# Kernel tuning notes

Measured on AMD Instinct MI355X. Metric: run time of the kernel, lower is better.

## Reference

```python
import jax, jax.numpy as jnp
import numpy as np
import math

B, C, H, W = 512, 64, 8, 8
E, NH, MEM = 64, 8, 8          # embed_dim, num_heads, mem_n
HD = E // NH                   # head_dim
THD = H * W * HD               # tot_head_dim = 512
AMB = 5.0                      # attn_mask_b
LN_EPS = 1e-5


def conv2d(x, w, b):
    y = jax.lax.conv_general_dilated(x, w, (1, 1), 'SAME',
                                     dimension_numbers=('NCHW', 'OIHW', 'NCHW'))
    return y + b[None, :, None, None]


def setup_inputs() -> dict:
    key = jax.random.key(0)
    ks = jax.random.split(key, 14)
    r = lambda k, s, sc=1.0: jax.random.normal(k, s, dtype=jnp.float32) * sc
    return {
        'input': r(ks[0], (B, C, H, W)),
        'h_cur': r(ks[1], (B, E, H, W)),
        'c_cur': r(ks[2], (B, E, H, W)),
        'concat_k': r(ks[3], (B, MEM, NH, THD)),
        'concat_v': r(ks[4], (B, MEM, NH, THD)),
        'attn_mask': jax.random.randint(ks[5], (B * NH, 1, MEM), 0, 2).astype(bool),
        'conv_w': r(ks[6], (5 * E, C + E, 3, 3), 0.05),
        'conv_b': jnp.zeros((5 * E,), jnp.float32),
        'proj_w': r(ks[7], (3 * E, C, 3, 3), 0.05),
        'proj_b': jnp.zeros((3 * E,), jnp.float32),
        'out_w': r(ks[8], (E, E, 3, 3), 0.05),
        'out_b': jnp.zeros((E,), jnp.float32),
        'ln_w': jnp.ones((E, H, W), jnp.float32),
        'ln_b': jnp.zeros((E, H, W), jnp.float32),
        'pos_w': r(ks[9], (MEM, H * W * E), 0.02),
        'pos_b': jax.random.uniform(ks[10], (MEM, NH), jnp.float32, -0.1, 0.1),
    }


def _cell(input, h_cur, c_cur, concat_k, concat_v, attn_mask,
          conv_w, conv_b, proj_w, proj_b, out_w, out_b, ln_w, ln_b, pos_w, pos_b):
    # ConvLSTM gates
    combined = jnp.concatenate([input, h_cur], axis=1)          # [B, C+E, H, W]
    cc = conv2d(combined, conv_w, conv_b)                       # [B, 5E, H, W]
    cc_i, cc_f, cc_o, cc_g, cc_a = jnp.split(cc, 5, axis=1)
    i = jax.nn.sigmoid(cc_i)
    f = jax.nn.sigmoid(cc_f)
    o = jax.nn.sigmoid(cc_o)
    g = jnp.tanh(cc_g)
    a = jax.nn.sigmoid(cc_a)
    c_next = f * c_cur + i * g

    # attention over growing memory
    kqv = conv2d(input, proj_w, proj_b)                         # [B, 3E, H, W]
    k, q, v = jnp.split(kqv, 3, axis=1)
    # [B, E, H, W] -> [B*NH, 1, THD] (contiguous split of E into NH heads)
    resh = lambda x: x.reshape(B * NH, 1, THD)
    k, q, v = resh(k), resh(q), resh(v)
    q_scaled = q / math.sqrt(THD)

    # prior memory: [B, MEM, NH, THD] -> [B*NH, MEM-1, THD]
    def mem_resh(m):
        return jnp.transpose(m[:, 1:], (1, 0, 2, 3)).reshape(MEM - 1, B * NH, THD).transpose(1, 0, 2)
    k_full = jnp.concatenate([mem_resh(concat_k), k], axis=1)   # [B*NH, MEM, THD]
    v_full = jnp.concatenate([mem_resh(concat_v), v], axis=1)

    # learned positional key offsets / score biases
    pos_w_e = jnp.broadcast_to(pos_w[:, None, :], (MEM, B, H * W * E)) \
                 .reshape(MEM, B * NH, THD).transpose(1, 0, 2)  # [B*NH, MEM, THD]
    pos_b_e = jnp.broadcast_to(pos_b[:, None, :], (MEM, B, NH)) \
                 .reshape(MEM, B * NH).T                        # [B*NH, MEM]
    k_full = k_full + pos_w_e

    # additive mask: -inf where masked, last slot forced to +attn_mask_b
    mask = jnp.where(attn_mask, -jnp.inf, 0.0).astype(q.dtype)  # [B*NH, 1, MEM]
    mask = mask.at[:, :, -1].set(AMB)

    scores = mask + jnp.einsum('bqd,bkd->bqk', q_scaled, k_full) + pos_b_e[:, None, :]
    w = jax.nn.softmax(scores, axis=-1)                         # [B*NH, 1, MEM]
    attn = jnp.einsum('bqk,bkd->bqd', w, v_full)                # [B*NH, 1, THD]
    attn = attn.reshape(B, E, H, W)

    out = conv2d(attn, out_w, out_b) + input[:, :E]
    # LayerNorm over (E, H, W)
    mu = jnp.mean(out, axis=(1, 2, 3), keepdims=True)
    var = jnp.mean((out - mu) ** 2, axis=(1, 2, 3), keepdims=True)
    out = (out - mu) / jnp.sqrt(var + LN_EPS) * ln_w[None] + ln_b[None]

    c_next = c_next + a * jnp.tanh(out)
    h_next = o * jnp.tanh(c_next)

    ret = lambda m: m.transpose(1, 0, 2).reshape(MEM, B, NH, THD).transpose(1, 0, 2, 3)
    return h_next, c_next, ret(k_full), ret(v_full)


def reference(input, h_cur, c_cur, concat_k, concat_v, attn_mask,
              conv_w, conv_b, proj_w, proj_b, out_w, out_b, ln_w, ln_b, pos_w, pos_b):
    return _cell(input, h_cur, c_cur, concat_k, concat_v, attn_mask,
                 conv_w, conv_b, proj_w, proj_b, out_w, out_b, ln_w, ln_b, pos_w, pos_b)
```

## Files before the change

kernel.cpp:

```cpp
#include <hip/hip_runtime.h>

typedef short short8 __attribute__((ext_vector_type(8)));
typedef __bf16 bf16x8 __attribute__((ext_vector_type(8)));
typedef float f32x4 __attribute__((ext_vector_type(4)));
typedef short s16x4 __attribute__((ext_vector_type(4)));
typedef unsigned u32x4 __attribute__((ext_vector_type(4)));

__device__ __forceinline__ short f2bf(float f) {
  unsigned u = __builtin_bit_cast(unsigned, f);
  u = (u + 0x7FFFu + ((u >> 16) & 1u)) >> 16;
  return (short)u;
}
__device__ __forceinline__ f32x4 mfma16(short8 a, short8 b, f32x4 c) {
  return __builtin_amdgcn_mfma_f32_16x16x32_bf16(
      __builtin_bit_cast(bf16x8, a), __builtin_bit_cast(bf16x8, b), c, 0, 0, 0);
}
__device__ __forceinline__ float sigm(float x) { return 1.0f / (1.0f + __expf(-x)); }
__device__ __forceinline__ float ftanh(float x) {
  return 1.0f - 2.0f / (1.0f + __expf(2.0f * x));
}
__device__ __forceinline__ f32x4 ld4(const float* p) { return *(const f32x4*)p; }
__device__ __forceinline__ void ntst4(float* p, f32x4 v) {
  __builtin_nontemporal_store(v, (f32x4*)p);
}

__global__ void pack_w(const float* __restrict__ w1, const float* __restrict__ w2,
                       const float* __restrict__ w3, short* __restrict__ out) {
  int e = blockIdx.x * 256 + threadIdx.x;
  if (e < 46080) {
    int kb8 = e / 320, n = e % 320;
    short8 v;
#pragma unroll
    for (int j = 0; j < 8; ++j) {
      int k = kb8 * 8 + j;
      int tap = k >> 7, ci = k & 127;
      v[j] = f2bf(w1[(n * 128 + ci) * 9 + tap]);
    }
    *(short8*)&out[e * 8] = v;
    return;
  }
  e -= 46080;
  if (e < 13824) {
    int kb8 = e / 192, n = e % 192;
    short8 v;
#pragma unroll
    for (int j = 0; j < 8; ++j) {
      int k = kb8 * 8 + j;
      int tap = k >> 6, ci = k & 63;
      v[j] = f2bf(w2[(n * 64 + ci) * 9 + tap]);
    }
    *(short8*)&out[(46080 + e) * 8] = v;
    return;
  }
  e -= 13824;
  {
    int kb8 = e / 64, n = e % 64;
    short8 v;
#pragma unroll
    for (int j = 0; j < 8; ++j) {
      int k = kb8 * 8 + j;
      int tap = k >> 6, ci = k & 63;
      v[j] = f2bf(w3[(n * 64 + ci) * 9 + tap]);
    }
    *(short8*)&out[(46080 + 13824 + e) * 8] = v;
  }
}

__launch_bounds__(512, 4)
__global__ void mid2_k(const float* __restrict__ input, const float* __restrict__ h_cur,
                       const float* __restrict__ c_cur, const float* __restrict__ ck,
                       const int* __restrict__ amask,
                       const float* __restrict__ conv_b, const float* __restrict__ proj_b,
                       const float* __restrict__ pos_w, const float* __restrict__ pos_b,
                       const short* __restrict__ pk1, const short* __restrict__ pk2,
                       float* __restrict__ o_k, float* __restrict__ o_v,
                       float* __restrict__ ws_wt, float* __restrict__ ws_ct,
                       unsigned* __restrict__ ws_oa) {
  __shared__ short comb[12800];
  __shared__ float Xb[4160];
  __shared__ float Vx[4160];
  __shared__ float sc_lds[8];
  float* combf = (float*)comb;
  unsigned* Xbu = (unsigned*)Xb;

  const int tid = threadIdx.x;
  const int wave = tid >> 6, lane = tid & 63;
  const int col = lane & 15, g4 = lane >> 4;
  const int wc = wave >> 1, wm = wave & 1;
  const int ch = wc * 16 + col;

  if (blockIdx.x < 512) {
    const int b = blockIdx.x;
    const int hd = wave;
    const int d0 = lane * 4, d1 = (lane + 64) * 4;
    if (tid < 8) sc_lds[tid] = 0.f;

#pragma unroll
    for (int i = 0; i < 2; ++i) {
      int idx = (tid + 512 * i) * 4;
      int c = idx >> 6, p0 = idx & 63;
      f32x4 vi = ld4(&input[b * 4096 + idx]);
#pragma unroll
      for (int j = 0; j < 4; ++j) {
        int p = p0 + j;
        int pp = ((p >> 3) + 1) * 10 + (p & 7) + 1;
        comb[pp * 64 + ((c + pp * 8) & 63)] = f2bf(vi[j]);
      }
    }
    for (int i = tid; i < 2304; i += 512) {
      int pr = i >> 6, c = i & 63;
      int pp = (pr < 10) ? pr
               : (pr < 20) ? (80 + pr)
               : (pr < 28) ? ((pr - 19) * 10)
                           : ((pr - 27) * 10 + 9);
      comb[pp * 64 + c] = 0;
    }
    __syncthreads();

    f32x4 acc2[2][3];
#pragma unroll
    for (int m = 0; m < 2; ++m)
#pragma unroll
      for (int g = 0; g < 3; ++g) acc2[m][g] = (f32x4){0.f, 0.f, 0.f, 0.f};
    short8 bb2[3];
#pragma unroll
    for (int g = 0; g < 3; ++g)
      bb2[g] = *(const short8*)&pk2[((g4)*192 + g * 64 + ch) * 8];
    for (int s = 0; s < 18; ++s) {
      short8 bbn[3];
      if (s < 17) {
        int kb8 = (s + 1) * 4 + g4;
#pragma unroll
        for (int g = 0; g < 3; ++g)
          bbn[g] = *(const short8*)&pk2[(kb8 * 192 + g * 64 + ch) * 8];
      }
      int tap = s >> 1, cib = s & 1;
      int kh = tap / 3, kw = tap % 3;
      short8 a[2];
#pragma unroll
      for (int m = 0; m < 2; ++m) {
        int p = (wm * 2 + m) * 16 + col;
        int pp = ((p >> 3) + kh) * 10 + (p & 7) + kw;
        int slot = (cib * 32 + g4 * 8 + pp * 8) & 63;
        a[m] = *(const short8*)&comb[pp * 64 + slot];
      }
#pragma unroll
      for (int m = 0; m < 2; ++m)
#pragma unroll
        for (int g = 0; g < 3; ++g) acc2[m][g] = mfma16(a[m], bb2[g], acc2[m][g]);
      if (s < 17) {
#pragma unroll
        for (int g = 0; g < 3; ++g) bb2[g] = bbn[g];
      }
    }

    float kreg[8], qreg[8], vreg[8], part7 = 0.f;
    {
      float pb0 = proj_b[ch], pb1 = proj_b[64 + ch], pb2 = proj_b[128 + ch];
      const float rsq = 0.044194173824159216f;
#pragma unroll
      for (int m = 0; m < 2; ++m)
#pragma unroll
        for (int r = 0; r < 4; ++r) {
          int p = (wm * 2 + m) * 16 + g4 * 4 + r;
          float kf = acc2[m][0][r] + pb0 + pos_w[7 * 4096 + ch * 64 + p];
          float qf = (acc2[m][1][r] + pb1) * rsq;
          float vf = acc2[m][2][r] + pb2;
          kreg[m * 4 + r] = kf;
          qreg[m * 4 + r] = qf;
          vreg[m * 4 + r] = vf;
          part7 = fmaf(qf, kf, part7);
        }
    }
    atomicAdd(&sc_lds[ch >> 3], part7);

    int msks[7];
    float pbv[7];
#pragma unroll
    for (int m = 0; m < 7; ++m) {
      msks[m] = amask[(b * 8 + hd) * 8 + m];
      pbv[m] = pos_b[m * 8 + hd];
    }

    __syncthreads();

#pragma unroll
    for (int m = 0; m < 2; ++m)
#pragma unroll
      for (int r = 0; r < 4; ++r) {
        int p = (wm * 2 + m) * 16 + g4 * 4 + r;
        combf[ch * 65 + p] = kreg[m * 4 + r];
        Xb[ch * 65 + p] = qreg[m * 4 + r];
        Vx[ch * 65 + p] = vreg[m * 4 + r];
      }
    __syncthreads();

    const size_t base7 = (size_t)(b * 64 + 56) * 512;
#pragma unroll
    for (int i = 0; i < 2; ++i) {
      int idx = (tid + 512 * i) * 4;
      int c = idx >> 6, p0 = idx & 63;
      f32x4 kq, vq;
#pragma unroll
      for (int j = 0; j < 4; ++j) {
        kq[j] = combf[c * 65 + p0 + j];
        vq[j] = Vx[c * 65 + p0 + j];
      }
      ntst4(&o_k[base7 + idx], kq);
      *(f32x4*)&o_v[base7 + idx] = vq;
    }
    const int cs0 = d0 >> 6, po0 = d0 & 63, cs1 = d1 >> 6, po1 = d1 & 63;
    f32x4 q0, q1;
#pragma unroll
    for (int j = 0; j < 4; ++j) {
      q0[j] = Xb[(hd * 8 + cs0) * 65 + po0 + j];
      q1[j] = Xb[(hd * 8 + cs1) * 65 + po1 + j];
    }
    float sc7 = sc_lds[hd] + pos_b[7 * 8 + hd] + 5.0f;

    float scv[8];
    scv[7] = sc7;
#pragma unroll
    for (int m = 0; m < 7; ++m) {
      const float* kp = ck + ((size_t)((b * 8 + m + 1) * 8 + hd)) * 512;
      const float* pw = pos_w + m * 4096 + hd * 512;
      f32x4 k0 = ld4(kp + d0) + ld4(pw + d0);
      f32x4 k1 = ld4(kp + d1) + ld4(pw + d1);
      float* dst = o_k + ((size_t)((b * 8 + m) * 8 + hd)) * 512;
      ntst4(dst + d0, k0);
      ntst4(dst + d1, k1);
      float part = 0.f;
#pragma unroll
      for (int j = 0; j < 4; ++j) {
        part = fmaf(q0[j], k0[j], part);
        part = fmaf(q1[j], k1[j], part);
      }
#pragma unroll
      for (int off = 32; off >= 1; off >>= 1) part += __shfl_xor(part, off);
      scv[m] = part + pbv[m] + (msks[m] ? -__builtin_inff() : 0.0f);
    }

    float mx = scv[0];
#pragma unroll
    for (int m = 1; m < 8; ++m) mx = fmaxf(mx, scv[m]);
    float w[8], s = 0.f;
#pragma unroll
    for (int m = 0; m < 8; ++m) {
      w[m] = __expf(scv[m] - mx);
      s += w[m];
    }
    float inv = 1.0f / s;
    if (lane == 0) {
#pragma unroll
      for (int m = 0; m < 8; ++m)
        ws_wt[(size_t)b * 64 + hd * 8 + m] = w[m] * inv;
    }
  } else {
    const int b = blockIdx.x - 512;
#pragma unroll
    for (int i = 0; i < 2; ++i) {
      int idx = (tid + 512 * i) * 4;
      int c = idx >> 6, p0 = idx & 63;
      f32x4 vi = ld4(&input[b * 4096 + idx]);
      f32x4 vh = ld4(&h_cur[b * 4096 + idx]);
      f32x4 vc = ld4(&c_cur[b * 4096 + idx]);
#pragma unroll
      for (int j = 0; j < 4; ++j) {
        int p = p0 + j;
        int pp = ((p >> 3) + 1) * 10 + (p & 7) + 1;
        comb[pp * 128 + ((c + pp * 8) & 127)] = f2bf(vi[j]);
        comb[pp * 128 + ((c + 64 + pp * 8) & 127)] = f2bf(vh[j]);
        Xb[c * 65 + p] = vc[j];
      }
    }
    for (int i = tid; i < 4608; i += 512) {
      int pr = i >> 7, c = i & 127;
      int pp = (pr < 10) ? pr
               : (pr < 20) ? (80 + pr)
               : (pr < 28) ? ((pr - 19) * 10)
                           : ((pr - 27) * 10 + 9);
      comb[pp * 128 + c] = 0;
    }
    __syncthreads();

    f32x4 acc1[2][5];
#pragma unroll
    for (int m = 0; m < 2; ++m)
#pragma unroll
      for (int g = 0; g < 5; ++g) acc1[m][g] = (f32x4){0.f, 0.f, 0.f, 0.f};
    short8 bb1[5];
#pragma unroll
    for (int g = 0; g < 5; ++g)
      bb1[g] = *(const short8*)&pk1[((g4)*320 + g * 64 + ch) * 8];
    for (int s = 0; s < 36; ++s) {
      short8 bbn[5];
      if (s < 35) {
        int kb8 = (s + 1) * 4 + g4;
#pragma unroll
        for (int g = 0; g < 5; ++g)
          bbn[g] = *(const short8*)&pk1[(kb8 * 320 + g * 64 + ch) * 8];
      }
      int tap = s >> 2, cib = s & 3;
      int kh = tap / 3, kw = tap % 3;
      short8 a[2];
#pragma unroll
      for (int m = 0; m < 2; ++m) {
        int p = (wm * 2 + m) * 16 + col;
        int pp = ((p >> 3) + kh) * 10 + (p & 7) + kw;
        int slot = (cib * 32 + g4 * 8 + pp * 8) & 127;
        a[m] = *(const short8*)&comb[pp * 128 + slot];
      }
#pragma unroll
      for (int m = 0; m < 2; ++m)
#pragma unroll
        for (int g = 0; g < 5; ++g) acc1[m][g] = mfma16(a[m], bb1[g], acc1[m][g]);
      if (s < 35) {
#pragma unroll
        for (int g = 0; g < 5; ++g) bb1[g] = bbn[g];
      }
    }

    float ctv[8];
    unsigned oav[8];
    {
      float bi0 = conv_b[ch], bi1 = conv_b[64 + ch], bi2 = conv_b[128 + ch];
      float bi3 = conv_b[192 + ch], bi4 = conv_b[256 + ch];
#pragma unroll
      for (int m = 0; m < 2; ++m)
#pragma unroll
        for (int r = 0; r < 4; ++r) {
          int p = (wm * 2 + m) * 16 + g4 * 4 + r;
          float iv = sigm(acc1[m][0][r] + bi0);
          float fv = sigm(acc1[m][1][r] + bi1);
          float ov = sigm(acc1[m][2][r] + bi2);
          float gv = ftanh(acc1[m][3][r] + bi3);
          float av = sigm(acc1[m][4][r] + bi4);
          ctv[m * 4 + r] = fv * Xb[ch * 65 + p] + iv * gv;
          oav[m * 4 + r] = ((unsigned)(unsigned short)f2bf(av) << 16) |
                           (unsigned)(unsigned short)f2bf(ov);
        }
    }
    __syncthreads();
#pragma unroll
    for (int m = 0; m < 2; ++m)
#pragma unroll
      for (int r = 0; r < 4; ++r) {
        int p = (wm * 2 + m) * 16 + g4 * 4 + r;
        combf[ch * 65 + p] = ctv[m * 4 + r];
        Xbu[ch * 65 + p] = oav[m * 4 + r];
      }
    __syncthreads();
#pragma unroll
    for (int i = 0; i < 2; ++i) {
      int idx = (tid + 512 * i) * 4;
      int c = idx >> 6, p0 = idx & 63;
      f32x4 cq;
      u32x4 oq;
#pragma unroll
      for (int j = 0; j < 4; ++j) {
        cq[j] = combf[c * 65 + p0 + j];
        oq[j] = Xbu[c * 65 + p0 + j];
      }
      *(f32x4*)&ws_ct[(size_t)b * 4096 + idx] = cq;
      *(u32x4*)&ws_oa[(size_t)b * 4096 + idx] = oq;
    }
  }
}

__launch_bounds__(512, 4)
__global__ void tail_k(const float* __restrict__ input, const float* __restrict__ cv,
                       const float* __restrict__ ws_wt,
                       const float* __restrict__ ws_ct,
                       const unsigned* __restrict__ ws_oa,
                       const float* __restrict__ out_b,
                       const float* __restrict__ ln_w, const float* __restrict__ ln_b,
                       const short* __restrict__ pk3,
                       float* __restrict__ o_h, float* __restrict__ o_c,
                       float* __restrict__ o_v) {
  __shared__ short comb[8320];
  __shared__ float Xb[4160];
  __shared__ float wt_s[64];
  __shared__ float red[16];
  float* combf = (float*)comb;
  unsigned* Xbu = (unsigned*)Xb;

  const int b = blockIdx.x;
  const int tid = threadIdx.x;
  const int wave = tid >> 6, lane = tid & 63;
  const int col = lane & 15, g4 = lane >> 4;
  const int wc = wave >> 1, wm = wave & 1;
  const int ch = wc * 16 + col;
  const int hd = wave;
  const int d0 = lane * 4, d1 = (lane + 64) * 4;

  f32x4 ctr[2];
  u32x4 oar[2];
#pragma unroll
  for (int i = 0; i < 2; ++i) {
    int idx = (tid + 512 * i) * 4;
    ctr[i] = ld4(&ws_ct[(size_t)b * 4096 + idx]);
    oar[i] = *(const u32x4*)&ws_oa[(size_t)b * 4096 + idx];
  }
  if (tid < 64) wt_s[tid] = ws_wt[(size_t)b * 64 + tid];

#pragma unroll
  for (int i = 0; i < 2; ++i) {
    int idx = (tid + 512 * i) * 4;
    int c = idx >> 6, p0 = idx & 63;
    f32x4 vi = ld4(&input[b * 4096 + idx]);
#pragma unroll
    for (int j = 0; j < 4; ++j) Xb[c * 65 + p0 + j] = vi[j];
  }
  for (int i = tid; i < 2304; i += 512) {
    int pr = i >> 6, c = i & 63;
    int pp = (pr < 10) ? pr
             : (pr < 20) ? (80 + pr)
             : (pr < 28) ? ((pr - 19) * 10)
                         : ((pr - 27) * 10 + 9);
    comb[pp * 64 + c] = 0;
  }
  __syncthreads();

  float wv[8];
#pragma unroll
  for (int m = 0; m < 8; ++m) wv[m] = wt_s[hd * 8 + m];

  f32x4 a0 = (f32x4){0.f, 0.f, 0.f, 0.f};
  f32x4 a1 = (f32x4){0.f, 0.f, 0.f, 0.f};
#pragma unroll
  for (int m = 0; m < 7; ++m) {
    const float* vp = cv + ((size_t)((b * 8 + m + 1) * 8 + hd)) * 512;
    f32x4 v0 = ld4(vp + d0);
    f32x4 v1 = ld4(vp + d1);
    float* dst = o_v + ((size_t)((b * 8 + m) * 8 + hd)) * 512;
    ntst4(dst + d0, v0);
    ntst4(dst + d1, v1);
    a0 += v0 * wv[m];
    a1 += v1 * wv[m];
  }
  {
    const float* vp = o_v + ((size_t)((b * 8 + 7) * 8 + hd)) * 512;
    a0 += ld4(vp + d0) * wv[7];
    a1 += ld4(vp + d1) * wv[7];
  }
#pragma unroll
  for (int j = 0; j < 4; ++j) {
    int dA = d0 + j, dB = d1 + j;
    int cA = hd * 8 + (dA >> 6), pA = dA & 63;
    int cB = hd * 8 + (dB >> 6), pB = dB & 63;
    int ppA = ((pA >> 3) + 1) * 10 + (pA & 7) + 1;
    int ppB = ((pB >> 3) + 1) * 10 + (pB & 7) + 1;
    comb[ppA * 64 + ((cA + ppA * 8) & 63)] = f2bf(a0[j]);
    comb[ppB * 64 + ((cB + ppB * 8) & 63)] = f2bf(a1[j]);
  }
  __syncthreads();

  f32x4 acc3[2];
  acc3[0] = (f32x4){0.f, 0.f, 0.f, 0.f};
  acc3[1] = (f32x4){0.f, 0.f, 0.f, 0.f};
  short8 bb3 = *(const short8*)&pk3[((g4)*64 + ch) * 8];
  for (int s = 0; s < 18; ++s) {
    short8 bbn;
    if (s < 17) {
      int kb8 = (s + 1) * 4 + g4;
      bbn = *(const short8*)&pk3[(kb8 * 64 + ch) * 8];
    }
    int tap = s >> 1, cib = s & 1;
    int kh = tap / 3, kw = tap % 3;
    short8 a[2];
#pragma unroll
    for (int m = 0; m < 2; ++m) {
      int p = (wm * 2 + m) * 16 + col;
      int pp = ((p >> 3) + kh) * 10 + (p & 7) + kw;
      int slot = (cib * 32 + g4 * 8 + pp * 8) & 63;
      a[m] = *(const short8*)&comb[pp * 64 + slot];
    }
#pragma unroll
    for (int m = 0; m < 2; ++m) acc3[m] = mfma16(a[m], bb3, acc3[m]);
    if (s < 17) bb3 = bbn;
  }

  float ov_[8], s1 = 0.f, s2 = 0.f;
  {
    float ob = out_b[ch];
#pragma unroll
    for (int m = 0; m < 2; ++m)
#pragma unroll
      for (int r = 0; r < 4; ++r) {
        int p = (wm * 2 + m) * 16 + g4 * 4 + r;
        float v = acc3[m][r] + ob + Xb[ch * 65 + p];
        ov_[m * 4 + r] = v;
        s1 += v;
        s2 += v * v;
      }
  }
#pragma unroll
  for (int off = 32; off >= 1; off >>= 1) {
    s1 += __shfl_xor(s1, off);
    s2 += __shfl_xor(s2, off);
  }
  if (lane == 0) { red[wave] = s1; red[8 + wave] = s2; }
  __syncthreads();
  float ts1 = 0.f, ts2 = 0.f;
#pragma unroll
  for (int w = 0; w < 8; ++w) { ts1 += red[w]; ts2 += red[8 + w]; }
  float mu = ts1 * (1.0f / 4096.0f);
  float var = ts2 * (1.0f / 4096.0f) - mu * mu;
  float rstd = rsqrtf(var + 1e-5f);

#pragma unroll
  for (int i = 0; i < 2; ++i) {
    int idx = (tid + 512 * i) * 4;
    int c = idx >> 6, p0 = idx & 63;
#pragma unroll
    for (int j = 0; j < 4; ++j) {
      combf[c * 65 + p0 + j] = ctr[i][j];
      Xbu[c * 65 + p0 + j] = oar[i][j];
    }
  }
  __syncthreads();

#pragma unroll
  for (int m = 0; m < 2; ++m)
#pragma unroll
    for (int r = 0; r < 4; ++r) {
      int p = (wm * 2 + m) * 16 + g4 * 4 + r;
      float ct = combf[ch * 65 + p];
      unsigned u = Xbu[ch * 65 + p];
      float og = __builtin_bit_cast(float, u << 16);
      float ag = __builtin_bit_cast(float, u & 0xffff0000u);
      float oln = (ov_[m * 4 + r] - mu) * rstd * ln_w[ch * 64 + p] + ln_b[ch * 64 + p];
      float cn = ct + ag * ftanh(oln);
      float hv = og * ftanh(cn);
      combf[ch * 65 + p] = hv;
      Xb[ch * 65 + p] = cn;
    }
  __syncthreads();
#pragma unroll
  for (int i = 0; i < 2; ++i) {
    int idx = (tid + 512 * i) * 4;
    int c = idx >> 6, p0 = idx & 63;
    f32x4 hq, cq;
#pragma unroll
    for (int j = 0; j < 4; ++j) {
      hq[j] = combf[c * 65 + p0 + j];
      cq[j] = Xb[c * 65 + p0 + j];
    }
    *(f32x4*)&o_h[b * 4096 + idx] = hq;
    *(f32x4*)&o_c[b * 4096 + idx] = cq;
  }
}

__launch_bounds__(512, 4)
__global__ void kqv_k(const float* __restrict__ input,
                      const float* __restrict__ proj_b,
                      const float* __restrict__ pos_w,
                      const short* __restrict__ pk2,
                      float* __restrict__ q_out, float* __restrict__ o_k,
                      float* __restrict__ o_v) {
  __shared__ short comb[6400];
  __shared__ float Xk[4160], Xq[4160], Xv[4160];
  const int b = blockIdx.x;
  const int tid = threadIdx.x;
  const int wave = tid >> 6, lane = tid & 63;
  const int col = lane & 15, g4 = lane >> 4;
  const int wc = wave >> 1, wm = wave & 1;
  const int ch = wc * 16 + col;
#pragma unroll
  for (int i = 0; i < 2; ++i) {
    int idx = (tid + 512 * i) * 4;
    int c = idx >> 6, p0 = idx & 63;
    f32x4 vi = ld4(&input[b * 4096 + idx]);
#pragma unroll
    for (int j = 0; j < 4; ++j) {
      int p = p0 + j;
      int pp = ((p >> 3) + 1) * 10 + (p & 7) + 1;
      comb[pp * 64 + ((c + pp * 8) & 63)] = f2bf(vi[j]);
    }
  }
  for (int i = tid; i < 2304; i += 512) {
    int pr = i >> 6, c = i & 63;
    int pp = (pr < 10) ? pr
             : (pr < 20) ? (80 + pr)
             : (pr < 28) ? ((pr - 19) * 10)
                         : ((pr - 27) * 10 + 9);
    comb[pp * 64 + c] = 0;
  }
  __syncthreads();
  f32x4 acc2[2][3];
#pragma unroll
  for (int m = 0; m < 2; ++m)
#pragma unroll
    for (int g = 0; g < 3; ++g) acc2[m][g] = (f32x4){0.f, 0.f, 0.f, 0.f};
  short8 bb2[3];
#pragma unroll
  for (int g = 0; g < 3; ++g)
    bb2[g] = *(const short8*)&pk2[((g4)*192 + g * 64 + ch) * 8];
  for (int s = 0; s < 18; ++s) {
    short8 bbn[3];
    if (s < 17) {
      int kb8 = (s + 1) * 4 + g4;
#pragma unroll
      for (int g = 0; g < 3; ++g)
        bbn[g] = *(const short8*)&pk2[(kb8 * 192 + g * 64 + ch) * 8];
    }
    int tap = s >> 1, cib = s & 1;
    int kh = tap / 3, kw = tap % 3;
    short8 a[2];
#pragma unroll
    for (int m = 0; m < 2; ++m) {
      int p = (wm * 2 + m) * 16 + col;
      int pp = ((p >> 3) + kh) * 10 + (p & 7) + kw;
      int slot = (cib * 32 + g4 * 8 + pp * 8) & 63;
      a[m] = *(const short8*)&comb[pp * 64 + slot];
    }
#pragma unroll
    for (int m = 0; m < 2; ++m)
#pragma unroll
      for (int g = 0; g < 3; ++g) acc2[m][g] = mfma16(a[m], bb2[g], acc2[m][g]);
    if (s < 17) {
#pragma unroll
      for (int g = 0; g < 3; ++g) bb2[g] = bbn[g];
    }
  }
  {
    float pb0 = proj_b[ch], pb1 = proj_b[64 + ch], pb2 = proj_b[128 + ch];
    const float rsq = 0.044194173824159216f;
#pragma unroll
    for (int m = 0; m < 2; ++m)
#pragma unroll
      for (int r = 0; r < 4; ++r) {
        int p = (wm * 2 + m) * 16 + g4 * 4 + r;
        Xk[ch * 65 + p] = acc2[m][0][r] + pb0 + pos_w[7 * 4096 + ch * 64 + p];
        Xq[ch * 65 + p] = (acc2[m][1][r] + pb1) * rsq;
        Xv[ch * 65 + p] = acc2[m][2][r] + pb2;
      }
  }
  __syncthreads();
  const size_t base7 = (size_t)(b * 64 + 56) * 512;
#pragma unroll
  for (int i = 0; i < 2; ++i) {
    int idx = (tid + 512 * i) * 4;
    int c = idx >> 6, p0 = idx & 63;
    f32x4 kq, qq, vq;
#pragma unroll
    for (int j = 0; j < 4; ++j) {
      kq[j] = Xk[c * 65 + p0 + j];
      qq[j] = Xq[c * 65 + p0 + j];
      vq[j] = Xv[c * 65 + p0 + j];
    }
    *(f32x4*)&o_k[base7 + idx] = kq;
    *(f32x4*)&q_out[(size_t)b * 4096 + idx] = qq;
    *(f32x4*)&o_v[base7 + idx] = vq;
  }
}

__launch_bounds__(64, 4)
__global__ void attn_k(const float* __restrict__ ck, const float* __restrict__ cv,
                       const int* __restrict__ amask,
                       const float* __restrict__ pos_w,
                       const float* __restrict__ pos_b,
                       const float* __restrict__ q_in,
                       float* __restrict__ o_k, float* __restrict__ o_v,
                       float* __restrict__ attn_out) {
  const int b = blockIdx.x >> 3;
  const int hd = blockIdx.x & 7;
  const int lane = threadIdx.x;
  const int d0 = lane * 4, d1 = (lane + 64) * 4;
  const float* qp = q_in + (size_t)b * 4096 + hd * 512;
  f32x4 q0 = ld4(qp + d0);
  f32x4 q1 = ld4(qp + d1);
  float sc[8];
#pragma unroll
  for (int m = 0; m < 7; ++m) {
    const float* kp = ck + ((size_t)((b * 8 + m + 1) * 8 + hd)) * 512;
    const float* pw = pos_w + m * 4096 + hd * 512;
    f32x4 k0 = ld4(kp + d0) + ld4(pw + d0);
    f32x4 k1 = ld4(kp + d1) + ld4(pw + d1);
    float* dst = o_k + ((size_t)((b * 8 + m) * 8 + hd)) * 512;
    ntst4(dst + d0, k0);
    ntst4(dst + d1, k1);
    float part = 0.f;
#pragma unroll
    for (int j = 0; j < 4; ++j) {
      part = fmaf(q0[j], k0[j], part);
      part = fmaf(q1[j], k1[j], part);
    }
#pragma unroll
    for (int off = 32; off >= 1; off >>= 1) part += __shfl_xor(part, off);
    float msk = amask[(b * 8 + hd) * 8 + m] ? -__builtin_inff() : 0.0f;
    sc[m] = part + pos_b[m * 8 + hd] + msk;
  }
  {
    const float* kp = o_k + ((size_t)((b * 8 + 7) * 8 + hd)) * 512;
    f32x4 k0 = ld4(kp + d0);
    f32x4 k1 = ld4(kp + d1);
    float part = 0.f;
#pragma unroll
    for (int j = 0; j < 4; ++j) {
      part = fmaf(q0[j], k0[j], part);
      part = fmaf(q1[j], k1[j], part);
    }
#pragma unroll
    for (int off = 32; off >= 1; off >>= 1) part += __shfl_xor(part, off);
    sc[7] = part + pos_b[7 * 8 + hd] + 5.0f;
  }
  float mx = sc[0];
#pragma unroll
  for (int m = 1; m < 8; ++m) mx = fmaxf(mx, sc[m]);
  float w[8], s = 0.f;
#pragma unroll
  for (int m = 0; m < 8; ++m) {
    w[m] = __expf(sc[m] - mx);
    s += w[m];
  }
  float inv = 1.0f / s;
#pragma unroll
  for (int m = 0; m < 8; ++m) w[m] *= inv;
  f32x4 a0 = (f32x4){0.f, 0.f, 0.f, 0.f};
  f32x4 a1 = (f32x4){0.f, 0.f, 0.f, 0.f};
#pragma unroll
  for (int m = 0; m < 7; ++m) {
    const float* vp = cv + ((size_t)((b * 8 + m + 1) * 8 + hd)) * 512;
    f32x4 v0 = ld4(vp + d0);
    f32x4 v1 = ld4(vp + d1);
    float* dst = o_v + ((size_t)((b * 8 + m) * 8 + hd)) * 512;
    ntst4(dst + d0, v0);
    ntst4(dst + d1, v1);
    a0 += v0 * w[m];
    a1 += v1 * w[m];
  }
  {
    const float* vp = o_v + ((size_t)((b * 8 + 7) * 8 + hd)) * 512;
    a0 += ld4(vp + d0) * w[7];
    a1 += ld4(vp + d1) * w[7];
  }
  float* ap = attn_out + (size_t)b * 4096 + hd * 512;
  *(f32x4*)&ap[d0] = a0;
  *(f32x4*)&ap[d1] = a1;
}

__launch_bounds__(512, 4)
__global__ void cell2_k(
    const float* __restrict__ input, const float* __restrict__ h_cur,
    const float* __restrict__ c_cur, const float* __restrict__ attn_in,
    const float* __restrict__ conv_b, const float* __restrict__ out_b,
    const float* __restrict__ ln_w, const float* __restrict__ ln_b,
    const short* __restrict__ pk1, const short* __restrict__ pk3,
    float* __restrict__ o_h, float* __restrict__ o_c) {
  __shared__ short comb[12800];
  __shared__ float Xb[4160];
  __shared__ float Qb[4160];
  __shared__ float Vb[4160];
  __shared__ float red[16];
  const int b = blockIdx.x;
  const int tid = threadIdx.x;
  const int wave = tid >> 6, lane = tid & 63;
  const int col = lane & 15, g4 = lane >> 4;
  const int wc = wave >> 1, wm = wave & 1;
  const int ch = wc * 16 + col;
#pragma unroll
  for (int i = 0; i < 2; ++i) {
    int idx = (tid + 512 * i) * 4;
    int c = idx >> 6, p0 = idx & 63;
    f32x4 vi = ld4(&input[b * 4096 + idx]);
    f32x4 vh = ld4(&h_cur[b * 4096 + idx]);
    f32x4 vc = ld4(&c_cur[b * 4096 + idx]);
#pragma unroll
    for (int j = 0; j < 4; ++j) {
      int p = p0 + j;
      int pp = ((p >> 3) + 1) * 10 + (p & 7) + 1;
      comb[pp * 128 + ((c + pp * 8) & 127)] = f2bf(vi[j]);
      comb[pp * 128 + ((c + 64 + pp * 8) & 127)] = f2bf(vh[j]);
      Xb[c * 65 + p] = vc[j];
    }
  }
  for (int i = tid; i < 4608; i += 512) {
    int pr = i >> 7, c = i & 127;
    int pp = (pr < 10) ? pr
             : (pr < 20) ? (80 + pr)
             : (pr < 28) ? ((pr - 19) * 10)
                         : ((pr - 27) * 10 + 9);
    comb[pp * 128 + c] = 0;
  }
  __syncthreads();
  f32x4 acc1[2][5];
#pragma unroll
  for (int m = 0; m < 2; ++m)
#pragma unroll
    for (int g = 0; g < 5; ++g) acc1[m][g] = (f32x4){0.f, 0.f, 0.f, 0.f};
  short8 bb1[5];
#pragma unroll
  for (int g = 0; g < 5; ++g)
    bb1[g] = *(const short8*)&pk1[((g4)*320 + g * 64 + ch) * 8];
  for (int s = 0; s < 36; ++s) {
    short8 bbn[5];
    if (s < 35) {
      int kb8 = (s + 1) * 4 + g4;
#pragma unroll
      for (int g = 0; g < 5; ++g)
        bbn[g] = *(const short8*)&pk1[(kb8 * 320 + g * 64 + ch) * 8];
    }
    int tap = s >> 2, cib = s & 3;
    int kh = tap / 3, kw = tap % 3;
    short8 a[2];
#pragma unroll
    for (int m = 0; m < 2; ++m) {
      int p = (wm * 2 + m) * 16 + col;
      int pp = ((p >> 3) + kh) * 10 + (p & 7) + kw;
      int slot = (cib * 32 + g4 * 8 + pp * 8) & 127;
      a[m] = *(const short8*)&comb[pp * 128 + slot];
    }
#pragma unroll
    for (int m = 0; m < 2; ++m)
#pragma unroll
      for (int g = 0; g < 5; ++g) acc1[m][g] = mfma16(a[m], bb1[g], acc1[m][g]);
    if (s < 35) {
#pragma unroll
      for (int g = 0; g < 5; ++g) bb1[g] = bbn[g];
    }
  }
  float ct_r[8], o_r[8], a_r[8];
  {
    float bi0 = conv_b[ch], bi1 = conv_b[64 + ch], bi2 = conv_b[128 + ch];
    float bi3 = conv_b[192 + ch], bi4 = conv_b[256 + ch];
#pragma unroll
    for (int m = 0; m < 2; ++m)
#pragma unroll
      for (int r = 0; r < 4; ++r) {
        int p = (wm * 2 + m) * 16 + g4 * 4 + r;
        float iv = sigm(acc1[m][0][r] + bi0);
        float fv = sigm(acc1[m][1][r] + bi1);
        float ov = sigm(acc1[m][2][r] + bi2);
        float gv = ftanh(acc1[m][3][r] + bi3);
        float av = sigm(acc1[m][4][r] + bi4);
        ct_r[m * 4 + r] = fv * Xb[ch * 65 + p] + iv * gv;
        o_r[m * 4 + r] = ov;
        a_r[m * 4 + r] = av;
      }
  }
  __syncthreads();
  {
    f32x4 av[2], iv[2];
#pragma unroll
    for (int i = 0; i < 2; ++i) {
      int idx = (tid + 512 * i) * 4;
      av[i] = ld4(&attn_in[b * 4096 + idx]);
      iv[i] = ld4(&input[b * 4096 + idx]);
    }
#pragma unroll
    for (int i = 0; i < 2; ++i) {
      int idx = (tid + 512 * i) * 4;
      int c = idx >> 6, p0 = idx & 63;
#pragma unroll
      for (int j = 0; j < 4; ++j) {
        int p = p0 + j;
        int pp = ((p >> 3) + 1) * 10 + (p & 7) + 1;
        comb[pp * 128 + ((c + pp * 8) & 127)] = f2bf(av[i][j]);
        Xb[c * 65 + p] = iv[i][j];
      }
    }
  }
  __syncthreads();
  f32x4 acc3[2];
  acc3[0] = (f32x4){0.f, 0.f, 0.f, 0.f};
  acc3[1] = (f32x4){0.f, 0.f, 0.f, 0.f};
  short8 bb3 = *(const short8*)&pk3[((g4)*64 + ch) * 8];
  for (int s = 0; s < 18; ++s) {
    short8 bbn;
    if (s < 17) {
      int kb8 = (s + 1) * 4 + g4;
      bbn = *(const short8*)&pk3[(kb8 * 64 + ch) * 8];
    }
    int tap = s >> 1, cib = s & 1;
    int kh = tap / 3, kw = tap % 3;
    short8 a[2];
#pragma unroll
    for (int m = 0; m < 2; ++m) {
      int p = (wm * 2 + m) * 16 + col;
      int pp = ((p >> 3) + kh) * 10 + (p & 7) + kw;
      int slot = (cib * 32 + g4 * 8 + pp * 8) & 127;
      a[m] = *(const short8*)&comb[pp * 128 + slot];
    }
#pragma unroll
    for (int m = 0; m < 2; ++m) acc3[m] = mfma16(a[m], bb3, acc3[m]);
    if (s < 17) bb3 = bbn;
  }
  float ov_[8], s1 = 0.f, s2 = 0.f;
  {
    float ob = out_b[ch];
#pragma unroll
    for (int m = 0; m < 2; ++m)
#pragma unroll
      for (int r = 0; r < 4; ++r) {
        int p = (wm * 2 + m) * 16 + g4 * 4 + r;
        float v = acc3[m][r] + ob + Xb[ch * 65 + p];
        ov_[m * 4 + r] = v;
        s1 += v;
        s2 += v * v;
      }
  }
#pragma unroll
  for (int off = 32; off >= 1; off >>= 1) {
    s1 += __shfl_xor(s1, off);
    s2 += __shfl_xor(s2, off);
  }
  if (lane == 0) { red[wave] = s1; red[8 + wave] = s2; }
  __syncthreads();
  float ts1 = 0.f, ts2 = 0.f;
#pragma unroll
  for (int w = 0; w < 8; ++w) { ts1 += red[w]; ts2 += red[8 + w]; }
  float mu = ts1 * (1.0f / 4096.0f);
  float var = ts2 * (1.0f / 4096.0f) - mu * mu;
  float rstd = rsqrtf(var + 1e-5f);
#pragma unroll
  for (int m = 0; m < 2; ++m)
#pragma unroll
    for (int r = 0; r < 4; ++r) {
      int p = (wm * 2 + m) * 16 + g4 * 4 + r;
      float oln = (ov_[m * 4 + r] - mu) * rstd * ln_w[ch * 64 + p] + ln_b[ch * 64 + p];
      float cn = ct_r[m * 4 + r] + a_r[m * 4 + r] * ftanh(oln);
      float hv = o_r[m * 4 + r] * ftanh(cn);
      Qb[ch * 65 + p] = hv;
      Vb[ch * 65 + p] = cn;
    }
  __syncthreads();
#pragma unroll
  for (int i = 0; i < 2; ++i) {
    int idx = (tid + 512 * i) * 4;
    int c = idx >> 6, p0 = idx & 63;
    f32x4 hv, cvv;
#pragma unroll
    for (int j = 0; j < 4; ++j) {
      hv[j] = Qb[c * 65 + p0 + j];
      cvv[j] = Vb[c * 65 + p0 + j];
    }
    *(f32x4*)&o_h[b * 4096 + idx] = hv;
    *(f32x4*)&o_c[b * 4096 + idx] = cvv;
  }
}

extern "C" void kernel_launch(void* const* d_in, const int* in_sizes, int n_in,
                              void* d_out, int out_size, void* d_ws, size_t ws_size,
                              hipStream_t stream) {
  (void)in_sizes; (void)n_in; (void)out_size;
  const float* input  = (const float*)d_in[0];
  const float* h_cur  = (const float*)d_in[1];
  const float* c_cur  = (const float*)d_in[2];
  const float* ck     = (const float*)d_in[3];
  const float* cv     = (const float*)d_in[4];
  const int*   amask  = (const int*)d_in[5];
  const float* conv_w = (const float*)d_in[6];
  const float* conv_b = (const float*)d_in[7];
  const float* proj_w = (const float*)d_in[8];
  const float* proj_b = (const float*)d_in[9];
  const float* out_w  = (const float*)d_in[10];
  const float* out_b  = (const float*)d_in[11];
  const float* ln_w   = (const float*)d_in[12];
  const float* ln_b   = (const float*)d_in[13];
  const float* pos_w  = (const float*)d_in[14];
  const float* pos_b  = (const float*)d_in[15];

  char* ws = (char*)d_ws;
  short* pk = (short*)ws;
  float* o_h = (float*)d_out;
  float* o_c = o_h + 2097152;
  float* o_k = o_h + 4194304;
  float* o_v = o_h + 20971520;

  pack_w<<<252, 256, 0, stream>>>(conv_w, proj_w, out_w, pk);

  if (ws_size >= (24u << 20)) {
    float* ws_wt = (float*)(ws + (2u << 20));
    float* ws_ct = (float*)(ws + (8u << 20));
    unsigned* ws_oa = (unsigned*)(ws + (16u << 20));
    mid2_k<<<1024, 512, 0, stream>>>(input, h_cur, c_cur, ck, amask,
                                     conv_b, proj_b, pos_w, pos_b,
                                     pk, pk + 368640,
                                     o_k, o_v, ws_wt, ws_ct, ws_oa);
    tail_k<<<512, 512, 0, stream>>>(input, cv, ws_wt, ws_ct, ws_oa,
                                    out_b, ln_w, ln_b, pk + 479232,
                                    o_h, o_c, o_v);
  } else {
    kqv_k<<<512, 512, 0, stream>>>(input, proj_b, pos_w, pk + 368640,
                                   o_h, o_k, o_v);
    attn_k<<<4096, 64, 0, stream>>>(ck, cv, amask, pos_w, pos_b, o_h,
                                    o_k, o_v, o_c);
    cell2_k<<<512, 512, 0, stream>>>(input, h_cur, c_cur, o_c,
                                     conv_b, out_b, ln_w, ln_b,
                                     pk, pk + 479232, o_h, o_c);
  }
}
```

Baseline: 99.34 us.

## Split mid kernel into three interleaved roles and move softmax to tail

The mid kernel now launches three block roles per batch (kqv/attention scores, ConvLSTM gates, and a dedicated V-history copy), interleaved by blockIdx modulo 3. The shifted V-history copy moves out of the tail kernel into its own role, and the softmax (mask, pos bias, normalization) moves into the tail kernel so mid only writes raw scores. The slot-7 K/V outputs are stored directly from registers instead of going through an LDS transpose, and K loads are batched before the shuffle reductions. This adds more blocks, lowers the launch-bounds occupancy hint, and raises the workspace threshold, which could push execution onto the fallback path if the workspace is small.

```diff
diff --git a/kernel.cpp b/kernel.cpp
--- a/kernel.cpp
+++ b/kernel.cpp
@@ -66,19 +66,18 @@
   }
 }
 
-__launch_bounds__(512, 4)
-__global__ void mid2_k(const float* __restrict__ input, const float* __restrict__ h_cur,
-                       const float* __restrict__ c_cur, const float* __restrict__ ck,
-                       const int* __restrict__ amask,
-                       const float* __restrict__ conv_b, const float* __restrict__ proj_b,
-                       const float* __restrict__ pos_w, const float* __restrict__ pos_b,
-                       const short* __restrict__ pk1, const short* __restrict__ pk2,
-                       float* __restrict__ o_k, float* __restrict__ o_v,
-                       float* __restrict__ ws_wt, float* __restrict__ ws_ct,
-                       unsigned* __restrict__ ws_oa) {
+__launch_bounds__(512, 2)
+__global__ void mid_k(const float* __restrict__ input, const float* __restrict__ h_cur,
+                      const float* __restrict__ c_cur, const float* __restrict__ ck,
+                      const float* __restrict__ cv,
+                      const float* __restrict__ conv_b, const float* __restrict__ proj_b,
+                      const float* __restrict__ pos_w,
+                      const short* __restrict__ pk1, const short* __restrict__ pk2,
+                      float* __restrict__ o_k, float* __restrict__ o_v,
+                      float* __restrict__ ws_sc, float* __restrict__ ws_ct,
+                      unsigned* __restrict__ ws_oa) {
   __shared__ short comb[12800];
   __shared__ float Xb[4160];
-  __shared__ float Vx[4160];
   __shared__ float sc_lds[8];
   float* combf = (float*)comb;
   unsigned* Xbu = (unsigned*)Xb;
@@ -88,11 +87,10 @@
   const int col = lane & 15, g4 = lane >> 4;
   const int wc = wave >> 1, wm = wave & 1;
   const int ch = wc * 16 + col;
-
-  if (blockIdx.x < 512) {
-    const int b = blockIdx.x;
-    const int hd = wave;
-    const int d0 = lane * 4, d1 = (lane + 64) * 4;
+  const int role = blockIdx.x % 3;
+  const int b = blockIdx.x / 3;
+
+  if (role == 0) {
     if (tid < 8) sc_lds[tid] = 0.f;
 
 #pragma unroll
@@ -154,61 +152,35 @@
       }
     }
 
-    float kreg[8], qreg[8], vreg[8], part7 = 0.f;
+    float part7 = 0.f;
     {
       float pb0 = proj_b[ch], pb1 = proj_b[64 + ch], pb2 = proj_b[128 + ch];
       const float rsq = 0.044194173824159216f;
-#pragma unroll
-      for (int m = 0; m < 2; ++m)
+      const size_t base7 = (size_t)(b * 8 + 7) * 4096;
+#pragma unroll
+      for (int m2 = 0; m2 < 2; ++m2) {
+        int p0 = wm * 32 + m2 * 16 + g4 * 4;
+        f32x4 pw7 = ld4(&pos_w[7 * 4096 + ch * 64 + p0]);
+        f32x4 kq, vq;
 #pragma unroll
         for (int r = 0; r < 4; ++r) {
-          int p = (wm * 2 + m) * 16 + g4 * 4 + r;
-          float kf = acc2[m][0][r] + pb0 + pos_w[7 * 4096 + ch * 64 + p];
-          float qf = (acc2[m][1][r] + pb1) * rsq;
-          float vf = acc2[m][2][r] + pb2;
-          kreg[m * 4 + r] = kf;
-          qreg[m * 4 + r] = qf;
-          vreg[m * 4 + r] = vf;
+          float kf = acc2[m2][0][r] + pb0 + pw7[r];
+          float qf = (acc2[m2][1][r] + pb1) * rsq;
+          float vf = acc2[m2][2][r] + pb2;
+          kq[r] = kf;
+          vq[r] = vf;
+          Xb[ch * 65 + p0 + r] = qf;
           part7 = fmaf(qf, kf, part7);
         }
+        *(f32x4*)&o_k[base7 + ch * 64 + p0] = kq;
+        *(f32x4*)&o_v[base7 + ch * 64 + p0] = vq;
+      }
     }
     atomicAdd(&sc_lds[ch >> 3], part7);
-
-    int msks[7];
-    float pbv[7];
-#pragma unroll
-    for (int m = 0; m < 7; ++m) {
-      msks[m] = amask[(b * 8 + hd) * 8 + m];
-      pbv[m] = pos_b[m * 8 + hd];
-    }
-
     __syncthreads();
 
-#pragma unroll
-    for (int m = 0; m < 2; ++m)
-#pragma unroll
-      for (int r = 0; r < 4; ++r) {
-        int p = (wm * 2 + m) * 16 + g4 * 4 + r;
-        combf[ch * 65 + p] = kreg[m * 4 + r];
-        Xb[ch * 65 + p] = qreg[m * 4 + r];
-        Vx[ch * 65 + p] = vreg[m * 4 + r];
-      }
-    __syncthreads();
-
-    const size_t base7 = (size_t)(b * 64 + 56) * 512;
-#pragma unroll
-    for (int i = 0; i < 2; ++i) {
-      int idx = (tid + 512 * i) * 4;
-      int c = idx >> 6, p0 = idx & 63;
-      f32x4 kq, vq;
-#pragma unroll
-      for (int j = 0; j < 4; ++j) {
-        kq[j] = combf[c * 65 + p0 + j];
-        vq[j] = Vx[c * 65 + p0 + j];
-      }
-      ntst4(&o_k[base7 + idx], kq);
-      *(f32x4*)&o_v[base7 + idx] = vq;
-    }
+    const int hd = wave;
+    const int d0 = lane * 4, d1 = (lane + 64) * 4;
     const int cs0 = d0 >> 6, po0 = d0 & 63, cs1 = d1 >> 6, po1 = d1 & 63;
     f32x4 q0, q1;
 #pragma unroll
@@ -216,47 +188,43 @@
       q0[j] = Xb[(hd * 8 + cs0) * 65 + po0 + j];
       q1[j] = Xb[(hd * 8 + cs1) * 65 + po1 + j];
     }
-    float sc7 = sc_lds[hd] + pos_b[7 * 8 + hd] + 5.0f;
-
-    float scv[8];
-    scv[7] = sc7;
+    float sc7raw = sc_lds[hd];
+
+    f32x4 ka[7], kb[7];
 #pragma unroll
     for (int m = 0; m < 7; ++m) {
-      const float* kp = ck + ((size_t)((b * 8 + m + 1) * 8 + hd)) * 512;
+      const float* src = ck + ((size_t)((b * 8 + m + 1) * 8 + hd)) * 512;
       const float* pw = pos_w + m * 4096 + hd * 512;
-      f32x4 k0 = ld4(kp + d0) + ld4(pw + d0);
-      f32x4 k1 = ld4(kp + d1) + ld4(pw + d1);
+      ka[m] = ld4(src + d0) + ld4(pw + d0);
+      kb[m] = ld4(src + d1) + ld4(pw + d1);
+    }
+    float part[7];
+#pragma unroll
+    for (int m = 0; m < 7; ++m) {
       float* dst = o_k + ((size_t)((b * 8 + m) * 8 + hd)) * 512;
-      ntst4(dst + d0, k0);
-      ntst4(dst + d1, k1);
-      float part = 0.f;
+      ntst4(dst + d0, ka[m]);
+      ntst4(dst + d1, kb[m]);
+      float pp = 0.f;
 #pragma unroll
       for (int j = 0; j < 4; ++j) {
-        part = fmaf(q0[j], k0[j], part);
-        part = fmaf(q1[j], k1[j], part);
-      }
-#pragma unroll
-      for (int off = 32; off >= 1; off >>= 1) part += __shfl_xor(part, off);
-      scv[m] = part + pbv[m] + (msks[m] ? -__builtin_inff() : 0.0f);
-    }
-
-    float mx = scv[0];
-#pragma unroll
-    for (int m = 1; m < 8; ++m) mx = fmaxf(mx, scv[m]);
-    float w[8], s = 0.f;
-#pragma unroll
-    for (int m = 0; m < 8; ++m) {
-      w[m] = __expf(scv[m] - mx);
-      s += w[m];
-    }
-    float inv = 1.0f / s;
+        pp = fmaf(q0[j], ka[m][j], pp);
+        pp = fmaf(q1[j], kb[m][j], pp);
+      }
+      part[m] = pp;
+    }
+#pragma unroll
+    for (int m = 0; m < 7; ++m) {
+#pragma unroll
+      for (int off = 32; off >= 1; off >>= 1)
+        part[m] += __shfl_xor(part[m], off);
+    }
     if (lane == 0) {
 #pragma unroll
-      for (int m = 0; m < 8; ++m)
-        ws_wt[(size_t)b * 64 + hd * 8 + m] = w[m] * inv;
-    }
-  } else {
-    const int b = blockIdx.x - 512;
+      for (int m = 0; m < 7; ++m)
+        ws_sc[(size_t)b * 64 + hd * 8 + m] = part[m];
+      ws_sc[(size_t)b * 64 + hd * 8 + 7] = sc7raw;
+    }
+  } else if (role == 1) {
 #pragma unroll
     for (int i = 0; i < 2; ++i) {
       int idx = (tid + 512 * i) * 4;
@@ -364,14 +332,27 @@
       *(f32x4*)&ws_ct[(size_t)b * 4096 + idx] = cq;
       *(u32x4*)&ws_oa[(size_t)b * 4096 + idx] = oq;
     }
+  } else {
+#pragma unroll
+    for (int m = 0; m < 7; ++m) {
+      const float* src = cv + (size_t)(b * 8 + m + 1) * 4096;
+      float* dst = o_v + (size_t)(b * 8 + m) * 4096;
+#pragma unroll
+      for (int i = 0; i < 2; ++i) {
+        int j = tid * 4 + i * 2048;
+        ntst4(dst + j, ld4(src + j));
+      }
+    }
   }
 }
 
 __launch_bounds__(512, 4)
 __global__ void tail_k(const float* __restrict__ input, const float* __restrict__ cv,
-                       const float* __restrict__ ws_wt,
+                       const float* __restrict__ ws_sc,
                        const float* __restrict__ ws_ct,
                        const unsigned* __restrict__ ws_oa,
+                       const int* __restrict__ amask,
+                       const float* __restrict__ pos_b,
                        const float* __restrict__ out_b,
                        const float* __restrict__ ln_w, const float* __restrict__ ln_b,
                        const short* __restrict__ pk3,
@@ -401,7 +382,27 @@
     ctr[i] = ld4(&ws_ct[(size_t)b * 4096 + idx]);
     oar[i] = *(const u32x4*)&ws_oa[(size_t)b * 4096 + idx];
   }
-  if (tid < 64) wt_s[tid] = ws_wt[(size_t)b * 64 + tid];
+  if (tid < 8) {
+    const int head = tid;
+    float scv[8];
+#pragma unroll
+    for (int m = 0; m < 7; ++m)
+      scv[m] = ws_sc[(size_t)b * 64 + head * 8 + m] + pos_b[m * 8 + head] +
+               (amask[(b * 8 + head) * 8 + m] ? -__builtin_inff() : 0.0f);
+    scv[7] = ws_sc[(size_t)b * 64 + head * 8 + 7] + pos_b[56 + head] + 5.0f;
+    float mx = scv[0];
+#pragma unroll
+    for (int m = 1; m < 8; ++m) mx = fmaxf(mx, scv[m]);
+    float w[8], s = 0.f;
+#pragma unroll
+    for (int m = 0; m < 8; ++m) {
+      w[m] = __expf(scv[m] - mx);
+      s += w[m];
+    }
+    float inv = 1.0f / s;
+#pragma unroll
+    for (int m = 0; m < 8; ++m) wt_s[head * 8 + m] = w[m] * inv;
+  }
 
 #pragma unroll
   for (int i = 0; i < 2; ++i) {
@@ -430,13 +431,8 @@
 #pragma unroll
   for (int m = 0; m < 7; ++m) {
     const float* vp = cv + ((size_t)((b * 8 + m + 1) * 8 + hd)) * 512;
-    f32x4 v0 = ld4(vp + d0);
-    f32x4 v1 = ld4(vp + d1);
-    float* dst = o_v + ((size_t)((b * 8 + m) * 8 + hd)) * 512;
-    ntst4(dst + d0, v0);
-    ntst4(dst + d1, v1);
-    a0 += v0 * wv[m];
-    a1 += v1 * wv[m];
+    a0 += ld4(vp + d0) * wv[m];
+    a1 += ld4(vp + d1) * wv[m];
   }
   {
     const float* vp = o_v + ((size_t)((b * 8 + 7) * 8 + hd)) * 512;
@@ -970,17 +966,17 @@
 
   pack_w<<<252, 256, 0, stream>>>(conv_w, proj_w, out_w, pk);
 
-  if (ws_size >= (24u << 20)) {
-    float* ws_wt = (float*)(ws + (2u << 20));
-    float* ws_ct = (float*)(ws + (8u << 20));
-    unsigned* ws_oa = (unsigned*)(ws + (16u << 20));
-    mid2_k<<<1024, 512, 0, stream>>>(input, h_cur, c_cur, ck, amask,
-                                     conv_b, proj_b, pos_w, pos_b,
-                                     pk, pk + 368640,
-                                     o_k, o_v, ws_wt, ws_ct, ws_oa);
-    tail_k<<<512, 512, 0, stream>>>(input, cv, ws_wt, ws_ct, ws_oa,
-                                    out_b, ln_w, ln_b, pk + 479232,
-                                    o_h, o_c, o_v);
+  if (ws_size >= (32u << 20)) {
+    float* ws_sc = (float*)(ws + (2u << 20));
+    float* ws_ct = (float*)(ws + (16u << 20));
+    unsigned* ws_oa = (unsigned*)(ws + (24u << 20));
+    mid_k<<<1536, 512, 0, stream>>>(input, h_cur, c_cur, ck, cv,
+                                    conv_b, proj_b, pos_w,
+                                    pk, pk + 368640,
+                                    o_k, o_v, ws_sc, ws_ct, ws_oa);
+    tail_k<<<512, 512, 0, stream>>>(input, cv, ws_sc, ws_ct, ws_oa,
+                                    amask, pos_b, out_b, ln_w, ln_b,
+                                    pk + 479232, o_h, o_c, o_v);
   } else {
     kqv_k<<<512, 512, 0, stream>>>(input, proj_b, pos_w, pk + 368640,
                                    o_h, o_k, o_v);
```

Result: slower. 102.8 us (+3.5%).

## Store kqv and gate outputs directly from accumulators, dropping LDS staging

Applied to the files above, without the earlier changes.

Writes the k/v slot-7 outputs and the c/o-a workspace values straight from MFMA accumulator registers as 16-byte vectors, instead of transposing through shared memory. Loads c_cur directly from global memory in the epilogue. Removes two shared buffers and some barriers, shrinking LDS use, and raises the launch-bounds occupancy hint. The trade is less coalesced global stores. The workspace offsets and the size threshold also change.

```diff
diff --git a/kernel.cpp b/kernel.cpp
--- a/kernel.cpp
+++ b/kernel.cpp
@@ -66,8 +66,8 @@
   }
 }
 
-__launch_bounds__(512, 4)
-__global__ void mid2_k(const float* __restrict__ input, const float* __restrict__ h_cur,
+__launch_bounds__(512, 8)
+__global__ void mid4_k(const float* __restrict__ input, const float* __restrict__ h_cur,
                        const float* __restrict__ c_cur, const float* __restrict__ ck,
                        const int* __restrict__ amask,
                        const float* __restrict__ conv_b, const float* __restrict__ proj_b,
@@ -77,11 +77,8 @@
                        float* __restrict__ ws_wt, float* __restrict__ ws_ct,
                        unsigned* __restrict__ ws_oa) {
   __shared__ short comb[12800];
-  __shared__ float Xb[4160];
-  __shared__ float Vx[4160];
   __shared__ float sc_lds[8];
   float* combf = (float*)comb;
-  unsigned* Xbu = (unsigned*)Xb;
 
   const int tid = threadIdx.x;
   const int wave = tid >> 6, lane = tid & 63;
@@ -91,8 +88,6 @@
 
   if (blockIdx.x < 512) {
     const int b = blockIdx.x;
-    const int hd = wave;
-    const int d0 = lane * 4, d1 = (lane + 64) * 4;
     if (tid < 8) sc_lds[tid] = 0.f;
 
 #pragma unroll
@@ -154,28 +149,35 @@
       }
     }
 
-    float kreg[8], qreg[8], vreg[8], part7 = 0.f;
+    float qreg[8], part7 = 0.f;
     {
       float pb0 = proj_b[ch], pb1 = proj_b[64 + ch], pb2 = proj_b[128 + ch];
       const float rsq = 0.044194173824159216f;
-#pragma unroll
-      for (int m = 0; m < 2; ++m)
+      const size_t base7 = (size_t)(b * 8 + 7) * 4096;
+#pragma unroll
+      for (int m2 = 0; m2 < 2; ++m2) {
+        int p0 = wm * 32 + m2 * 16 + g4 * 4;
+        f32x4 pw7 = ld4(&pos_w[7 * 4096 + ch * 64 + p0]);
+        f32x4 kq, vq;
 #pragma unroll
         for (int r = 0; r < 4; ++r) {
-          int p = (wm * 2 + m) * 16 + g4 * 4 + r;
-          float kf = acc2[m][0][r] + pb0 + pos_w[7 * 4096 + ch * 64 + p];
-          float qf = (acc2[m][1][r] + pb1) * rsq;
-          float vf = acc2[m][2][r] + pb2;
-          kreg[m * 4 + r] = kf;
-          qreg[m * 4 + r] = qf;
-          vreg[m * 4 + r] = vf;
+          float kf = acc2[m2][0][r] + pb0 + pw7[r];
+          float qf = (acc2[m2][1][r] + pb1) * rsq;
+          float vf = acc2[m2][2][r] + pb2;
+          kq[r] = kf;
+          vq[r] = vf;
+          qreg[m2 * 4 + r] = qf;
           part7 = fmaf(qf, kf, part7);
         }
+        *(f32x4*)&o_k[base7 + ch * 64 + p0] = kq;
+        *(f32x4*)&o_v[base7 + ch * 64 + p0] = vq;
+      }
     }
     atomicAdd(&sc_lds[ch >> 3], part7);
 
     int msks[7];
     float pbv[7];
+    const int hd = wave;
 #pragma unroll
     for (int m = 0; m < 7; ++m) {
       msks[m] = amask[(b * 8 + hd) * 8 + m];
@@ -185,36 +187,20 @@
     __syncthreads();
 
 #pragma unroll
-    for (int m = 0; m < 2; ++m)
-#pragma unroll
-      for (int r = 0; r < 4; ++r) {
-        int p = (wm * 2 + m) * 16 + g4 * 4 + r;
-        combf[ch * 65 + p] = kreg[m * 4 + r];
-        Xb[ch * 65 + p] = qreg[m * 4 + r];
-        Vx[ch * 65 + p] = vreg[m * 4 + r];
-      }
+    for (int m2 = 0; m2 < 2; ++m2) {
+      int p0 = wm * 32 + m2 * 16 + g4 * 4;
+#pragma unroll
+      for (int r = 0; r < 4; ++r) combf[ch * 65 + p0 + r] = qreg[m2 * 4 + r];
+    }
     __syncthreads();
 
-    const size_t base7 = (size_t)(b * 64 + 56) * 512;
-#pragma unroll
-    for (int i = 0; i < 2; ++i) {
-      int idx = (tid + 512 * i) * 4;
-      int c = idx >> 6, p0 = idx & 63;
-      f32x4 kq, vq;
-#pragma unroll
-      for (int j = 0; j < 4; ++j) {
-        kq[j] = combf[c * 65 + p0 + j];
-        vq[j] = Vx[c * 65 + p0 + j];
-      }
-      ntst4(&o_k[base7 + idx], kq);
-      *(f32x4*)&o_v[base7 + idx] = vq;
-    }
+    const int d0 = lane * 4, d1 = (lane + 64) * 4;
     const int cs0 = d0 >> 6, po0 = d0 & 63, cs1 = d1 >> 6, po1 = d1 & 63;
     f32x4 q0, q1;
 #pragma unroll
     for (int j = 0; j < 4; ++j) {
-      q0[j] = Xb[(hd * 8 + cs0) * 65 + po0 + j];
-      q1[j] = Xb[(hd * 8 + cs1) * 65 + po1 + j];
+      q0[j] = combf[(hd * 8 + cs0) * 65 + po0 + j];
+      q1[j] = combf[(hd * 8 + cs1) * 65 + po1 + j];
     }
     float sc7 = sc_lds[hd] + pos_b[7 * 8 + hd] + 5.0f;
 
@@ -263,14 +249,12 @@
       int c = idx >> 6, p0 = idx & 63;
       f32x4 vi = ld4(&input[b * 4096 + idx]);
       f32x4 vh = ld4(&h_cur[b * 4096 + idx]);
-      f32x4 vc = ld4(&c_cur[b * 4096 + idx]);
 #pragma unroll
       for (int j = 0; j < 4; ++j) {
         int p = p0 + j;
         int pp = ((p >> 3) + 1) * 10 + (p & 7) + 1;
         comb[pp * 128 + ((c + pp * 8) & 127)] = f2bf(vi[j]);
         comb[pp * 128 + ((c + 64 + pp * 8) & 127)] = f2bf(vh[j]);
-        Xb[c * 65 + p] = vc[j];
       }
     }
     for (int i = tid; i < 4608; i += 512) {
@@ -320,49 +304,29 @@
       }
     }
 
-    float ctv[8];
-    unsigned oav[8];
     {
       float bi0 = conv_b[ch], bi1 = conv_b[64 + ch], bi2 = conv_b[128 + ch];
       float bi3 = conv_b[192 + ch], bi4 = conv_b[256 + ch];
 #pragma unroll
-      for (int m = 0; m < 2; ++m)
+      for (int m2 = 0; m2 < 2; ++m2) {
+        int p0 = wm * 32 + m2 * 16 + g4 * 4;
+        f32x4 cr = ld4(&c_cur[(size_t)b * 4096 + ch * 64 + p0]);
+        f32x4 cq;
+        u32x4 oq;
 #pragma unroll
         for (int r = 0; r < 4; ++r) {
-          int p = (wm * 2 + m) * 16 + g4 * 4 + r;
-          float iv = sigm(acc1[m][0][r] + bi0);
-          float fv = sigm(acc1[m][1][r] + bi1);
-          float ov = sigm(acc1[m][2][r] + bi2);
-          float gv = ftanh(acc1[m][3][r] + bi3);
-          float av = sigm(acc1[m][4][r] + bi4);
-          ctv[m * 4 + r] = fv * Xb[ch * 65 + p] + iv * gv;
-          oav[m * 4 + r] = ((unsigned)(unsigned short)f2bf(av) << 16) |
-                           (unsigned)(unsigned short)f2bf(ov);
+          float iv = sigm(acc1[m2][0][r] + bi0);
+          float fv = sigm(acc1[m2][1][r] + bi1);
+          float ov = sigm(acc1[m2][2][r] + bi2);
+          float gv = ftanh(acc1[m2][3][r] + bi3);
+          float av = sigm(acc1[m2][4][r] + bi4);
+          cq[r] = fv * cr[r] + iv * gv;
+          oq[r] = ((unsigned)(unsigned short)f2bf(av) << 16) |
+                  (unsigned)(unsigned short)f2bf(ov);
         }
-    }
-    __syncthreads();
-#pragma unroll
-    for (int m = 0; m < 2; ++m)
-#pragma unroll
-      for (int r = 0; r < 4; ++r) {
-        int p = (wm * 2 + m) * 16 + g4 * 4 + r;
-        combf[ch * 65 + p] = ctv[m * 4 + r];
-        Xbu[ch * 65 + p] = oav[m * 4 + r];
-      }
-    __syncthreads();
-#pragma unroll
-    for (int i = 0; i < 2; ++i) {
-      int idx = (tid + 512 * i) * 4;
-      int c = idx >> 6, p0 = idx & 63;
-      f32x4 cq;
-      u32x4 oq;
-#pragma unroll
-      for (int j = 0; j < 4; ++j) {
-        cq[j] = combf[c * 65 + p0 + j];
-        oq[j] = Xbu[c * 65 + p0 + j];
-      }
-      *(f32x4*)&ws_ct[(size_t)b * 4096 + idx] = cq;
-      *(u32x4*)&ws_oa[(size_t)b * 4096 + idx] = oq;
+        *(f32x4*)&ws_ct[(size_t)b * 4096 + ch * 64 + p0] = cq;
+        *(u32x4*)&ws_oa[(size_t)b * 4096 + ch * 64 + p0] = oq;
+      }
     }
   }
 }
@@ -970,11 +934,11 @@
 
   pack_w<<<252, 256, 0, stream>>>(conv_w, proj_w, out_w, pk);
 
-  if (ws_size >= (24u << 20)) {
+  if (ws_size >= (32u << 20)) {
     float* ws_wt = (float*)(ws + (2u << 20));
-    float* ws_ct = (float*)(ws + (8u << 20));
-    unsigned* ws_oa = (unsigned*)(ws + (16u << 20));
-    mid2_k<<<1024, 512, 0, stream>>>(input, h_cur, c_cur, ck, amask,
+    float* ws_ct = (float*)(ws + (16u << 20));
+    unsigned* ws_oa = (unsigned*)(ws + (24u << 20));
+    mid4_k<<<1024, 512, 0, stream>>>(input, h_cur, c_cur, ck, amask,
                                      conv_b, proj_b, pos_w, pos_b,
                                      pk, pk + 368640,
                                      o_k, o_v, ws_wt, ws_ct, ws_oa);
```

Measured after the change: 206.6 us. 108% more time.
